# Optimization experiments

Hardware: AMD Instinct MI355X
Metric: run time of the kernel (lower is better)

Reference implementation:

```python
import jax, jax.numpy as jnp
import numpy as np

# Architecture constants (from init_kwargs; reversible halves d_model)
D_MODEL = 1024
D_INNER = D_MODEL // 2          # 512, width of attn/MLP inside reversible block
NUM_HEADS = 8
HEAD_DIM = D_INNER // NUM_HEADS  # 64
SEGMENT_LENGTHS = (512, 1024)
DILATION_RATES = (1, 2)
HIDDEN = 2 * D_INNER             # MLP hidden_layer_multiplier=2


def layer_norm(x, g, b, eps=1e-5):
    m = jnp.mean(x, axis=-1, keepdims=True)
    v = jnp.var(x, axis=-1, keepdims=True)
    return (x - m) * jax.lax.rsqrt(v + eps) * g + b


def dilated_attention(q, k, v):
    """LongNet dilated attention. q,k,v: [b, n, h, dh]. Heads are partitioned
    evenly across (segment_length, dilation_rate) configs; within each config,
    tokens at positions offset::r inside each segment attend to each other."""
    b, n, h, dh = q.shape
    num_groups = len(SEGMENT_LENGTHS)
    gsize = h // num_groups
    scale = 1.0 / np.sqrt(dh).astype(np.float32)
    out = jnp.zeros_like(q)
    for i, (s, r) in enumerate(zip(SEGMENT_LENGTHS, DILATION_RATES)):
        off = i % r
        h0 = i * gsize
        # positions selected by this config: [n_seg, s//r]
        pos = jnp.arange(n // s)[:, None] * s + off + r * jnp.arange(s // r)[None, :]

        def pick(x):
            xs = x[:, :, h0:h0 + gsize, :]      # [b, n, g, dh]
            return xs[:, pos]                   # [b, n_seg, s//r, g, dh]

        qi, ki, vi = pick(q), pick(k), pick(v)
        scores = jnp.einsum('bnqgd,bnkgd->bngqk', qi, ki) * scale
        attn = jax.nn.softmax(scores, axis=-1)
        oi = jnp.einsum('bngqk,bnkgd->bnqgd', attn, vi)
        out = out.at[:, pos.reshape(-1), h0:h0 + gsize, :].set(
            oi.reshape(b, -1, gsize, dh))
    return out


def mhda(x, Wq, bq, Wk, bk, Wv, bv, Wo, bo):
    b, n, d = x.shape
    q = (x @ Wq + bq).reshape(b, n, NUM_HEADS, HEAD_DIM)
    k = (x @ Wk + bk).reshape(b, n, NUM_HEADS, HEAD_DIM)
    v = (x @ Wv + bv).reshape(b, n, NUM_HEADS, HEAD_DIM)
    o = dilated_attention(q, k, v).reshape(b, n, d)
    return o @ Wo + bo


def setup_inputs() -> dict:
    key = jax.random.key(0)
    ks = jax.random.split(key, 8)
    d, hdn = D_INNER, HIDDEN
    w = lambda k, *sh: (jax.random.normal(k, sh, dtype=jnp.float32) * 0.02)
    return {
        'x': jax.random.normal(ks[0], (4, 8192, D_MODEL), dtype=jnp.float32),
        'ln1_g': jnp.ones((d,), jnp.float32), 'ln1_b': jnp.zeros((d,), jnp.float32),
        'Wq': w(ks[1], d, d), 'bq': jnp.zeros((d,), jnp.float32),
        'Wk': w(ks[2], d, d), 'bk': jnp.zeros((d,), jnp.float32),
        'Wv': w(ks[3], d, d), 'bv': jnp.zeros((d,), jnp.float32),
        'Wo': w(ks[4], d, d), 'bo': jnp.zeros((d,), jnp.float32),
        'ln2_g': jnp.ones((d,), jnp.float32), 'ln2_b': jnp.zeros((d,), jnp.float32),
        'W1': w(ks[5], d, hdn), 'b1': jnp.zeros((hdn,), jnp.float32),
        'W2': w(ks[6], hdn, d), 'b2': jnp.zeros((d,), jnp.float32),
    }


def reference(x, ln1_g, ln1_b, Wq, bq, Wk, bk, Wv, bv, Wo, bo,
              ln2_g, ln2_b, W1, b1, W2, b2):
    # Reversible residual block (forward math): split channels in half,
    # y1 = x1 + Attn(LN(x2)); y2 = x2 + MLP(LN(y1)); concat.
    x1, x2 = jnp.split(x, 2, axis=-1)
    y1 = x1 + mhda(layer_norm(x2, ln1_g, ln1_b), Wq, bq, Wk, bk, Wv, bv, Wo, bo)
    h = layer_norm(y1, ln2_g, ln2_b)
    y2 = x2 + jax.nn.relu(h @ W1 + b1) @ W2 + b2
    return jnp.concatenate([y1, y2], axis=-1)
```

## Files before the change

### kernel.cpp

```cpp
#include <hip/hip_runtime.h>
#include <hip/hip_bf16.h>

typedef unsigned short ushort_t;
typedef __bf16 bf16x8 __attribute__((ext_vector_type(8)));
typedef float f32x4 __attribute__((ext_vector_type(4)));
typedef short s16x8 __attribute__((ext_vector_type(8)));

__device__ __forceinline__ float b2f(ushort_t u) {
    union { unsigned u; float f; } x;
    x.u = ((unsigned)u) << 16;
    return x.f;
}
__device__ __forceinline__ ushort_t f2b(float f) {
    union { float f; unsigned u; } x;
    x.f = f;
    unsigned r = x.u + 0x7fffu + ((x.u >> 16) & 1u);
    return (ushort_t)(r >> 16);
}

__device__ __forceinline__ void glds16(const ushort_t* g, ushort_t* l) {
    __builtin_amdgcn_global_load_lds(
        (const __attribute__((address_space(1))) void*)g,
        (__attribute__((address_space(3))) void*)l, 16, 0, 0);
}

__global__ void transpose_k(const float* __restrict__ src, ushort_t* __restrict__ dst,
                            int R, int C) {
    long i = (long)blockIdx.x * 256 + threadIdx.x;
    if (i < (long)R * C) {
        int c = (int)(i / R);
        int r = (int)(i % R);
        dst[i] = f2b(src[(long)r * C + c]);
    }
}

__global__ void concat3_k(const float* a, const float* b, const float* c,
                          float* dst, int n) {
    int i = blockIdx.x * 256 + threadIdx.x;
    if (i < 3 * n) dst[i] = (i < n) ? a[i] : (i < 2 * n ? b[i - n] : c[i - 2 * n]);
}

__global__ __launch_bounds__(256) void ln_kernel(
    const float* __restrict__ x, long xstride,
    const float* __restrict__ g, const float* __restrict__ be,
    ushort_t* __restrict__ out, long ostride) {
    int r = blockIdx.x, t = threadIdx.x;
    const float* row = x + (long)r * xstride;
    float2 p = *(const float2*)(row + 2 * t);
    float v0 = p.x, v1 = p.y;
    float s = v0 + v1, ss = v0 * v0 + v1 * v1;
#pragma unroll
    for (int off = 32; off; off >>= 1) {
        s += __shfl_xor(s, off, 64);
        ss += __shfl_xor(ss, off, 64);
    }
    __shared__ float sb[8];
    int w = t >> 6;
    if ((t & 63) == 0) { sb[w] = s; sb[4 + w] = ss; }
    __syncthreads();
    s = sb[0] + sb[1] + sb[2] + sb[3];
    ss = sb[4] + sb[5] + sb[6] + sb[7];
    float mean = s * (1.f / 512.f);
    float var = ss * (1.f / 512.f) - mean * mean;
    float rstd = rsqrtf(var + 1e-5f);
    float2 gp = *(const float2*)(g + 2 * t);
    float2 bp = *(const float2*)(be + 2 * t);
    ushort2 q;
    q.x = f2b((v0 - mean) * rstd * gp.x + bp.x);
    q.y = f2b((v1 - mean) * rstd * gp.y + bp.y);
    *(ushort2*)(out + (long)r * ostride + 2 * t) = q;
}

__global__ __launch_bounds__(256) void gemm_kernel(
    const ushort_t* __restrict__ A, const ushort_t* __restrict__ Bt,
    const float* __restrict__ bias,
    const float* __restrict__ res, long res_stride,
    void* __restrict__ outp, long out_stride, int out_is_f32,
    int K, int relu) {
    __shared__ __align__(16) ushort_t lA[128 * 32];
    __shared__ __align__(16) ushort_t lB[128 * 32];
    const int t = threadIdx.x;
    const int m0 = blockIdx.x * 128, n0 = blockIdx.y * 128;
    const int wave = t >> 6, lane = t & 63, quad = lane >> 4, l16 = lane & 15;
    const int wm = (wave & 1) * 64, wn = (wave >> 1) * 64;
    f32x4 acc[4][4];
#pragma unroll
    for (int i = 0; i < 4; i++)
#pragma unroll
        for (int j = 0; j < 4; j++) acc[i][j] = (f32x4){0.f, 0.f, 0.f, 0.f};

    const int srow = t >> 2;
    const int scol = (t & 3) * 8;
    const ushort_t* gA0 = A + (long)(m0 + srow) * K + scol;
    const ushort_t* gA1 = gA0 + (long)64 * K;
    const ushort_t* gB0 = Bt + (long)(n0 + srow) * K + scol;
    const ushort_t* gB1 = gB0 + (long)64 * K;
    ushort_t* lA0 = lA + wave * 512;
    ushort_t* lB0 = lB + wave * 512;

    for (int k0 = 0; k0 < K; k0 += 32) {
        __syncthreads();
        glds16(gA0 + k0, lA0);
        glds16(gA1 + k0, lA0 + 2048);
        glds16(gB0 + k0, lB0);
        glds16(gB1 + k0, lB0 + 2048);
        __syncthreads();
        bf16x8 af[4], bfr[4];
#pragma unroll
        for (int i = 0; i < 4; i++) {
            af[i] = *(const bf16x8*)&lA[(wm + i * 16 + l16) * 32 + quad * 8];
            bfr[i] = *(const bf16x8*)&lB[(wn + i * 16 + l16) * 32 + quad * 8];
        }
#pragma unroll
        for (int i = 0; i < 4; i++)
#pragma unroll
            for (int j = 0; j < 4; j++)
                acc[i][j] = __builtin_amdgcn_mfma_f32_16x16x32_bf16(af[i], bfr[j], acc[i][j], 0, 0, 0);
    }
#pragma unroll
    for (int i = 0; i < 4; i++) {
#pragma unroll
        for (int r = 0; r < 4; r++) {
            long row = m0 + wm + i * 16 + quad * 4 + r;
#pragma unroll
            for (int j = 0; j < 4; j++) {
                int col = n0 + wn + j * 16 + l16;
                float v = acc[i][j][r] + bias[col];
                if (res) v += res[row * res_stride + col];
                if (relu) v = fmaxf(v, 0.f);
                if (out_is_f32)
                    ((float*)outp)[row * out_stride + col] = v;
                else
                    ((ushort_t*)outp)[row * out_stride + col] = f2b(v);
            }
        }
    }
}

__global__ __launch_bounds__(256) void attn_kernel(const ushort_t* __restrict__ qkv,
                                                   ushort_t* __restrict__ o) {
    __shared__ __align__(16) ushort_t lK[64 * 72];
    __shared__ __align__(16) ushort_t lV[64 * 72];
    __shared__ __align__(16) ushort_t lP[4 * 32 * 72];

    const int bid = blockIdx.x;
    const int t = threadIdx.x;
    int grp, b, h, seg, qblk;
    if (bid < 1024) {
        grp = 0; qblk = bid & 3; seg = (bid >> 2) & 15; h = (bid >> 6) & 3; b = bid >> 8;
    } else {
        int u = bid - 1024;
        grp = 1; qblk = u & 3; seg = (u >> 2) & 7; h = (u >> 5) & 3; b = u >> 7;
    }
    const int habs = grp * 4 + h;
    const long segbase = (grp == 0) ? (long)seg * 512 : (long)seg * 1024 + 1;
    const int stok = 1 + grp;
    const long btok = (long)b * 8192;
    const int q0 = qblk * 128;

    const int wave = t >> 6, lane = t & 63, quad = lane >> 4, l16 = lane & 15;
    ushort_t* lPw = lP + wave * 32 * 72;

    bf16x8 qf[2][2];
#pragma unroll
    for (int m = 0; m < 2; m++) {
        long tok = btok + segbase + (long)stok * (q0 + wave * 32 + m * 16 + l16);
        const ushort_t* qp = qkv + tok * 1536 + habs * 64;
        qf[m][0] = *(const bf16x8*)(qp + quad * 8);
        qf[m][1] = *(const bf16x8*)(qp + 32 + quad * 8);
    }

    f32x4 oacc[2][4];
#pragma unroll
    for (int m = 0; m < 2; m++)
#pragma unroll
        for (int n = 0; n < 4; n++) oacc[m][n] = (f32x4){0.f, 0.f, 0.f, 0.f};
    float mst[2][4], lst[2][4];
#pragma unroll
    for (int m = 0; m < 2; m++)
#pragma unroll
        for (int r = 0; r < 4; r++) { mst[m][r] = -1e30f; lst[m][r] = 0.f; }

    const int skey = t >> 2;
    const int sdg = t & 3;

    for (int c = 0; c < 8; c++) {
        long ktok = btok + segbase + (long)stok * (c * 64 + skey);
        const ushort_t* kp = qkv + ktok * 1536 + 512 + habs * 64 + sdg * 16;
        s16x8 kr0 = *(const s16x8*)kp;
        s16x8 kr1 = *(const s16x8*)(kp + 8);
        s16x8 vr0 = *(const s16x8*)(kp + 512);
        s16x8 vr1 = *(const s16x8*)(kp + 520);
        __syncthreads();
        *(s16x8*)&lK[skey * 72 + sdg * 16] = kr0;
        *(s16x8*)&lK[skey * 72 + sdg * 16 + 8] = kr1;
#pragma unroll
        for (int i = 0; i < 8; i++) {
            int d0 = sdg * 16 + i, d1 = sdg * 16 + 8 + i;
            lV[d0 * 72 + (skey ^ (((d0 >> 3) & 7) * 8))] = (ushort_t)vr0[i];
            lV[d1 * 72 + (skey ^ (((d1 >> 3) & 7) * 8))] = (ushort_t)vr1[i];
        }
        __syncthreads();

#pragma unroll
        for (int m = 0; m < 2; m++) {
            f32x4 sa[4];
#pragma unroll
            for (int n = 0; n < 4; n++) sa[n] = (f32x4){0.f, 0.f, 0.f, 0.f};
#pragma unroll
            for (int ks = 0; ks < 2; ks++)
#pragma unroll
                for (int n = 0; n < 4; n++) {
                    bf16x8 kf = *(const bf16x8*)&lK[(n * 16 + l16) * 72 + ks * 32 + quad * 8];
                    sa[n] = __builtin_amdgcn_mfma_f32_16x16x32_bf16(qf[m][ks], kf, sa[n], 0, 0, 0);
                }
#pragma unroll
            for (int r = 0; r < 4; r++) {
                float mx = fmaxf(fmaxf(sa[0][r], sa[1][r]), fmaxf(sa[2][r], sa[3][r]));
                mx = fmaxf(mx, __shfl_xor(mx, 1, 64));
                mx = fmaxf(mx, __shfl_xor(mx, 2, 64));
                mx = fmaxf(mx, __shfl_xor(mx, 4, 64));
                mx = fmaxf(mx, __shfl_xor(mx, 8, 64));
                mx *= 0.125f;
                float mold = mst[m][r];
                float mnew = fmaxf(mold, mx);
                float alpha = __expf(mold - mnew);
                float rsum = 0.f;
#pragma unroll
                for (int n = 0; n < 4; n++) {
                    float p = __expf(fmaf(sa[n][r], 0.125f, -mnew));
                    rsum += p;
                    sa[n][r] = p;
                }
                rsum += __shfl_xor(rsum, 1, 64);
                rsum += __shfl_xor(rsum, 2, 64);
                rsum += __shfl_xor(rsum, 4, 64);
                rsum += __shfl_xor(rsum, 8, 64);
                lst[m][r] = lst[m][r] * alpha + rsum;
                mst[m][r] = mnew;
#pragma unroll
                for (int n = 0; n < 4; n++) oacc[m][n][r] *= alpha;
            }
#pragma unroll
            for (int r = 0; r < 4; r++)
#pragma unroll
                for (int n = 0; n < 4; n++)
                    lPw[(m * 16 + quad * 4 + r) * 72 + n * 16 + l16] = f2b(sa[n][r]);
        }
        __asm__ volatile("s_waitcnt lgkmcnt(0)" ::: "memory");

#pragma unroll
        for (int m = 0; m < 2; m++) {
            bf16x8 pf[2];
#pragma unroll
            for (int ks = 0; ks < 2; ks++)
                pf[ks] = *(const bf16x8*)&lPw[(m * 16 + l16) * 72 + ks * 32 + quad * 8];
#pragma unroll
            for (int n = 0; n < 4; n++) {
                int shift = ((n * 2 + (l16 >> 3)) & 7) * 8;
#pragma unroll
                for (int ks = 0; ks < 2; ks++) {
                    int kcol = (ks * 32 + quad * 8) ^ shift;
                    bf16x8 vf = *(const bf16x8*)&lV[(n * 16 + l16) * 72 + kcol];
                    oacc[m][n] = __builtin_amdgcn_mfma_f32_16x16x32_bf16(pf[ks], vf, oacc[m][n], 0, 0, 0);
                }
            }
        }
    }

#pragma unroll
    for (int m = 0; m < 2; m++) {
#pragma unroll
        for (int r = 0; r < 4; r++) {
            float inv = 1.f / lst[m][r];
            long tok = btok + segbase + (long)stok * (q0 + wave * 32 + m * 16 + quad * 4 + r);
            ushort_t* op = o + tok * 512 + habs * 64;
#pragma unroll
            for (int n = 0; n < 4; n++) op[n * 16 + l16] = f2b(oacc[m][n][r] * inv);
        }
    }
}

extern "C" void kernel_launch(void* const* d_in, const int* in_sizes, int n_in,
                              void* d_out, int out_size, void* d_ws, size_t ws_size,
                              hipStream_t stream) {
    const float* x    = (const float*)d_in[0];
    const float* ln1g = (const float*)d_in[1];
    const float* ln1b = (const float*)d_in[2];
    const float* Wq   = (const float*)d_in[3];
    const float* bq   = (const float*)d_in[4];
    const float* Wk   = (const float*)d_in[5];
    const float* bk   = (const float*)d_in[6];
    const float* Wv   = (const float*)d_in[7];
    const float* bv   = (const float*)d_in[8];
    const float* Wo   = (const float*)d_in[9];
    const float* bo   = (const float*)d_in[10];
    const float* ln2g = (const float*)d_in[11];
    const float* ln2b = (const float*)d_in[12];
    const float* W1   = (const float*)d_in[13];
    const float* b1   = (const float*)d_in[14];
    const float* W2   = (const float*)d_in[15];
    const float* b2   = (const float*)d_in[16];
    float* out = (float*)d_out;
    char* ws = (char*)d_ws;

    const size_t NEED = 134217728ull + 1572864 + 524288 + 1048576 + 1048576 + 8192;
    if (ws_size < NEED) return;

    ushort_t* XN    = (ushort_t*)(ws + 0);
    ushort_t* QKV   = (ushort_t*)(ws + 33554432);
    ushort_t* O     = XN;
    ushort_t* H     = XN;
    ushort_t* ACT   = QKV;
    ushort_t* WQKVT = (ushort_t*)(ws + 134217728);
    ushort_t* WOT   = WQKVT + 786432;
    ushort_t* W1T   = WOT + 262144;
    ushort_t* W2T   = W1T + 524288;
    float*    BQKV  = (float*)(W2T + 524288);

    transpose_k<<<1024, 256, 0, stream>>>(Wq, WQKVT, 512, 512);
    transpose_k<<<1024, 256, 0, stream>>>(Wk, WQKVT + 262144, 512, 512);
    transpose_k<<<1024, 256, 0, stream>>>(Wv, WQKVT + 524288, 512, 512);
    transpose_k<<<1024, 256, 0, stream>>>(Wo, WOT, 512, 512);
    transpose_k<<<2048, 256, 0, stream>>>(W1, W1T, 512, 1024);
    transpose_k<<<2048, 256, 0, stream>>>(W2, W2T, 1024, 512);
    concat3_k<<<6, 256, 0, stream>>>(bq, bk, bv, BQKV, 512);

    ln_kernel<<<32768, 256, 0, stream>>>(x + 512, 1024, ln1g, ln1b, XN, 512);
    gemm_kernel<<<dim3(256, 12), 256, 0, stream>>>(XN, WQKVT, BQKV, nullptr, 0,
                                                   QKV, 1536, 0, 512, 0);
    hipMemsetAsync(O, 0, 33554432, stream);
    attn_kernel<<<1536, 256, 0, stream>>>(QKV, O);
    gemm_kernel<<<dim3(256, 4), 256, 0, stream>>>(O, WOT, bo, x, 1024,
                                                  out, 1024, 1, 512, 0);
    ln_kernel<<<32768, 256, 0, stream>>>(out, 1024, ln2g, ln2b, H, 512);
    gemm_kernel<<<dim3(256, 8), 256, 0, stream>>>(H, W1T, b1, nullptr, 0,
                                                  ACT, 1024, 0, 512, 1);
    gemm_kernel<<<dim3(256, 4), 256, 0, stream>>>(ACT, W2T, b2, x + 512, 1024,
                                                  out + 512, 1024, 1, 1024, 0);
}
```

Before: 793.7 us.

## Pipeline GEMM LDS loads with 5-slot ring buffer and vmcnt waits

Replaces the single-buffer load/sync/compute loop in the GEMM kernel with a 5-slot LDS ring. Four K-tiles are prefetched ahead through global_load_lds, and each iteration uses explicit s_waitcnt vmcnt counts plus one barrier. The aim is to hide global memory latency behind MFMA work and to remove one of the two barriers per K step. It raises LDS use to 80KB per block, which may cut occupancy, and it depends on the exact vmcnt bookkeeping being right.

```diff
diff --git a/kernel.cpp b/kernel.cpp
--- a/kernel.cpp
+++ b/kernel.cpp
@@ -77,8 +77,8 @@
     const float* __restrict__ res, long res_stride,
     void* __restrict__ outp, long out_stride, int out_is_f32,
     int K, int relu) {
-    __shared__ __align__(16) ushort_t lA[128 * 32];
-    __shared__ __align__(16) ushort_t lB[128 * 32];
+    __shared__ __align__(16) ushort_t lA[5][128 * 32];
+    __shared__ __align__(16) ushort_t lB[5][128 * 32];
     const int t = threadIdx.x;
     const int m0 = blockIdx.x * 128, n0 = blockIdx.y * 128;
     const int wave = t >> 6, lane = t & 63, quad = lane >> 4, l16 = lane & 15;
@@ -95,21 +95,49 @@
     const ushort_t* gA1 = gA0 + (long)64 * K;
     const ushort_t* gB0 = Bt + (long)(n0 + srow) * K + scol;
     const ushort_t* gB1 = gB0 + (long)64 * K;
-    ushort_t* lA0 = lA + wave * 512;
-    ushort_t* lB0 = lB + wave * 512;
-
-    for (int k0 = 0; k0 < K; k0 += 32) {
-        __syncthreads();
-        glds16(gA0 + k0, lA0);
-        glds16(gA1 + k0, lA0 + 2048);
-        glds16(gB0 + k0, lB0);
-        glds16(gB1 + k0, lB0 + 2048);
-        __syncthreads();
+    const int lofs = wave * 512;
+
+#define ISSUE_TILE(slot, k0)                          \
+    do {                                              \
+        glds16(gA0 + (k0), &lA[slot][lofs]);          \
+        glds16(gA1 + (k0), &lA[slot][lofs + 2048]);   \
+        glds16(gB0 + (k0), &lB[slot][lofs]);          \
+        glds16(gB1 + (k0), &lB[slot][lofs + 2048]);   \
+    } while (0)
+
+    const int T = K >> 5;
+    ISSUE_TILE(0, 0);
+    ISSUE_TILE(1, 32);
+    ISSUE_TILE(2, 64);
+    ISSUE_TILE(3, 96);
+
+    int pr = 0, pw = 4;
+    for (int tt = 0; tt < T; ++tt) {
+        if (tt < T - 3)
+            asm volatile("s_waitcnt vmcnt(12)" ::: "memory");
+        else if (tt == T - 3)
+            asm volatile("s_waitcnt vmcnt(8)" ::: "memory");
+        else if (tt == T - 2)
+            asm volatile("s_waitcnt vmcnt(4)" ::: "memory");
+        else
+            asm volatile("s_waitcnt vmcnt(0)" ::: "memory");
+        __builtin_amdgcn_s_barrier();
+        asm volatile("" ::: "memory");
+
+        if (tt + 4 < T) {
+            ISSUE_TILE(pw, (tt + 4) * 32);
+            pw = (pw == 4) ? 0 : pw + 1;
+        }
+
+        const ushort_t* la = lA[pr];
+        const ushort_t* lb = lB[pr];
+        pr = (pr == 4) ? 0 : pr + 1;
+
         bf16x8 af[4], bfr[4];
 #pragma unroll
         for (int i = 0; i < 4; i++) {
-            af[i] = *(const bf16x8*)&lA[(wm + i * 16 + l16) * 32 + quad * 8];
-            bfr[i] = *(const bf16x8*)&lB[(wn + i * 16 + l16) * 32 + quad * 8];
+            af[i]  = *(const bf16x8*)&la[(wm + i * 16 + l16) * 32 + quad * 8];
+            bfr[i] = *(const bf16x8*)&lb[(wn + i * 16 + l16) * 32 + quad * 8];
         }
 #pragma unroll
         for (int i = 0; i < 4; i++)
@@ -117,6 +145,8 @@
             for (int j = 0; j < 4; j++)
                 acc[i][j] = __builtin_amdgcn_mfma_f32_16x16x32_bf16(af[i], bfr[j], acc[i][j], 0, 0, 0);
     }
+#undef ISSUE_TILE
+
 #pragma unroll
     for (int i = 0; i < 4; i++) {
 #pragma unroll
```

Result: slower. 819.9 us (+3.3%).

## Widen GEMM tiles to 128x512 with double-buffered LDS prefetch

Applied to the files above, without the earlier changes.

The GEMM kernel moves to 512 threads and a 128x512 output tile, with each wave computing a 64x128 sub-tile. Global-to-LDS loads for the next K-step are issued into a second buffer while the current one is consumed, replacing the two barriers per step with one wait and one barrier. This is meant to reuse each A tile across more columns and hide load latency behind MFMA work. In exchange the grid drops to 256-768 blocks, and the 32 accumulators per thread raise register pressure, which may limit occupancy and load balance on a chip with many CUs.

```diff
diff --git a/kernel.cpp b/kernel.cpp
--- a/kernel.cpp
+++ b/kernel.cpp
@@ -71,59 +71,74 @@
     *(ushort2*)(out + (long)r * ostride + 2 * t) = q;
 }
 
-__global__ __launch_bounds__(256) void gemm_kernel(
+__global__ __launch_bounds__(512, 2) void gemm_kernel(
     const ushort_t* __restrict__ A, const ushort_t* __restrict__ Bt,
     const float* __restrict__ bias,
     const float* __restrict__ res, long res_stride,
     void* __restrict__ outp, long out_stride, int out_is_f32,
     int K, int relu) {
-    __shared__ __align__(16) ushort_t lA[128 * 32];
-    __shared__ __align__(16) ushort_t lB[128 * 32];
+    __shared__ __align__(16) ushort_t lA[2][128 * 32];
+    __shared__ __align__(16) ushort_t lB[2][512 * 32];
     const int t = threadIdx.x;
-    const int m0 = blockIdx.x * 128, n0 = blockIdx.y * 128;
+    const int m0 = blockIdx.x * 128, n0 = blockIdx.y * 512;
     const int wave = t >> 6, lane = t & 63, quad = lane >> 4, l16 = lane & 15;
-    const int wm = (wave & 1) * 64, wn = (wave >> 1) * 64;
-    f32x4 acc[4][4];
+    const int wm = (wave & 1) * 64, wn = (wave >> 1) * 128;
+    f32x4 acc[4][8];
 #pragma unroll
     for (int i = 0; i < 4; i++)
 #pragma unroll
-        for (int j = 0; j < 4; j++) acc[i][j] = (f32x4){0.f, 0.f, 0.f, 0.f};
+        for (int j = 0; j < 8; j++) acc[i][j] = (f32x4){0.f, 0.f, 0.f, 0.f};
 
     const int srow = t >> 2;
     const int scol = (t & 3) * 8;
-    const ushort_t* gA0 = A + (long)(m0 + srow) * K + scol;
-    const ushort_t* gA1 = gA0 + (long)64 * K;
+    const ushort_t* gA  = A  + (long)(m0 + srow) * K + scol;
     const ushort_t* gB0 = Bt + (long)(n0 + srow) * K + scol;
-    const ushort_t* gB1 = gB0 + (long)64 * K;
-    ushort_t* lA0 = lA + wave * 512;
-    ushort_t* lB0 = lB + wave * 512;
-
-    for (int k0 = 0; k0 < K; k0 += 32) {
-        __syncthreads();
-        glds16(gA0 + k0, lA0);
-        glds16(gA1 + k0, lA0 + 2048);
-        glds16(gB0 + k0, lB0);
-        glds16(gB1 + k0, lB0 + 2048);
-        __syncthreads();
-        bf16x8 af[4], bfr[4];
-#pragma unroll
-        for (int i = 0; i < 4; i++) {
-            af[i] = *(const bf16x8*)&lA[(wm + i * 16 + l16) * 32 + quad * 8];
-            bfr[i] = *(const bf16x8*)&lB[(wn + i * 16 + l16) * 32 + quad * 8];
-        }
+    const ushort_t* gB1 = gB0 + (long)128 * K;
+    const ushort_t* gB2 = gB0 + (long)256 * K;
+    const ushort_t* gB3 = gB0 + (long)384 * K;
+    const int lofs = wave * 512;
+
+#define ISSUE_TILE(sl, k0)                              \
+    do {                                                \
+        glds16(gA  + (k0), &lA[sl][lofs]);              \
+        glds16(gB0 + (k0), &lB[sl][lofs]);              \
+        glds16(gB1 + (k0), &lB[sl][4096 + lofs]);       \
+        glds16(gB2 + (k0), &lB[sl][8192 + lofs]);       \
+        glds16(gB3 + (k0), &lB[sl][12288 + lofs]);      \
+    } while (0)
+
+    const int T = K >> 5;
+    ISSUE_TILE(0, 0);
+    int sl = 0;
+    for (int tt = 0; tt < T; ++tt) {
+        asm volatile("s_waitcnt vmcnt(0)" ::: "memory");
+        __builtin_amdgcn_s_barrier();
+        asm volatile("" ::: "memory");
+        if (tt + 1 < T) ISSUE_TILE(sl ^ 1, (tt + 1) * 32);
+        const ushort_t* la = lA[sl];
+        const ushort_t* lb = lB[sl];
+        sl ^= 1;
+        bf16x8 af[4];
 #pragma unroll
         for (int i = 0; i < 4; i++)
-#pragma unroll
-            for (int j = 0; j < 4; j++)
-                acc[i][j] = __builtin_amdgcn_mfma_f32_16x16x32_bf16(af[i], bfr[j], acc[i][j], 0, 0, 0);
-    }
+            af[i] = *(const bf16x8*)&la[(wm + i * 16 + l16) * 32 + quad * 8];
+#pragma unroll
+        for (int j = 0; j < 8; j++) {
+            bf16x8 bfv = *(const bf16x8*)&lb[(wn + j * 16 + l16) * 32 + quad * 8];
+#pragma unroll
+            for (int i = 0; i < 4; i++)
+                acc[i][j] = __builtin_amdgcn_mfma_f32_16x16x32_bf16(af[i], bfv, acc[i][j], 0, 0, 0);
+        }
+    }
+#undef ISSUE_TILE
+
 #pragma unroll
     for (int i = 0; i < 4; i++) {
 #pragma unroll
         for (int r = 0; r < 4; r++) {
             long row = m0 + wm + i * 16 + quad * 4 + r;
 #pragma unroll
-            for (int j = 0; j < 4; j++) {
+            for (int j = 0; j < 8; j++) {
                 int col = n0 + wn + j * 16 + l16;
                 float v = acc[i][j][r] + bias[col];
                 if (res) v += res[row * res_stride + col];
@@ -327,15 +342,15 @@
     concat3_k<<<6, 256, 0, stream>>>(bq, bk, bv, BQKV, 512);
 
     ln_kernel<<<32768, 256, 0, stream>>>(x + 512, 1024, ln1g, ln1b, XN, 512);
-    gemm_kernel<<<dim3(256, 12), 256, 0, stream>>>(XN, WQKVT, BQKV, nullptr, 0,
-                                                   QKV, 1536, 0, 512, 0);
+    gemm_kernel<<<dim3(256, 3), 512, 0, stream>>>(XN, WQKVT, BQKV, nullptr, 0,
+                                                  QKV, 1536, 0, 512, 0);
     hipMemsetAsync(O, 0, 33554432, stream);
     attn_kernel<<<1536, 256, 0, stream>>>(QKV, O);
-    gemm_kernel<<<dim3(256, 4), 256, 0, stream>>>(O, WOT, bo, x, 1024,
+    gemm_kernel<<<dim3(256, 1), 512, 0, stream>>>(O, WOT, bo, x, 1024,
                                                   out, 1024, 1, 512, 0);
     ln_kernel<<<32768, 256, 0, stream>>>(out, 1024, ln2g, ln2b, H, 512);
-    gemm_kernel<<<dim3(256, 8), 256, 0, stream>>>(H, W1T, b1, nullptr, 0,
+    gemm_kernel<<<dim3(256, 2), 512, 0, stream>>>(H, W1T, b1, nullptr, 0,
                                                   ACT, 1024, 0, 512, 1);
-    gemm_kernel<<<dim3(256, 4), 256, 0, stream>>>(ACT, W2T, b2, x + 512, 1024,
+    gemm_kernel<<<dim3(256, 1), 512, 0, stream>>>(ACT, W2T, b2, x + 512, 1024,
                                                   out + 512, 1024, 1, 1024, 0);
 }
```

New measurement: 817.8 us. +3.0%, slower.

## Double-buffer GEMM LDS tiles and remap blocks for XCD-local reuse

Applied to the files above, without the earlier changes.

The GEMM kernel now double-buffers its LDS tiles. The global-to-LDS load for the next K step is issued right after the barrier, so it overlaps the MFMA work on the current tile, and the loop needs one barrier per step instead of two. The launch grid is flattened to 1D and block IDs are remapped so that each XCD (bid&7) handles a contiguous run of M tiles and walks all N tiles, which is meant to improve L2 reuse of the A rows. Launch bounds now request 5 waves per SIMD, and LDS use per block doubles to 32KB, which could limit occupancy.

```diff
diff --git a/kernel.cpp b/kernel.cpp
--- a/kernel.cpp
+++ b/kernel.cpp
@@ -71,16 +71,23 @@
     *(ushort2*)(out + (long)r * ostride + 2 * t) = q;
 }
 
-__global__ __launch_bounds__(256) void gemm_kernel(
+__global__ __launch_bounds__(256, 5) void gemm_kernel(
     const ushort_t* __restrict__ A, const ushort_t* __restrict__ Bt,
     const float* __restrict__ bias,
     const float* __restrict__ res, long res_stride,
     void* __restrict__ outp, long out_stride, int out_is_f32,
-    int K, int relu) {
-    __shared__ __align__(16) ushort_t lA[128 * 32];
-    __shared__ __align__(16) ushort_t lB[128 * 32];
+    int K, int relu, int nTiles) {
+    __shared__ __align__(16) ushort_t lA[2][128 * 32];
+    __shared__ __align__(16) ushort_t lB[2][128 * 32];
     const int t = threadIdx.x;
-    const int m0 = blockIdx.x * 128, n0 = blockIdx.y * 128;
+    const int bid = blockIdx.x;
+    const int xcd = bid & 7;
+    const int jj = bid >> 3;
+    const int mPerXcd = (int)gridDim.x / (nTiles * 8);
+    const int mt = xcd * mPerXcd + jj / nTiles;
+    const int nt = jj % nTiles;
+    const int m0 = mt * 128, n0 = nt * 128;
+
     const int wave = t >> 6, lane = t & 63, quad = lane >> 4, l16 = lane & 15;
     const int wm = (wave & 1) * 64, wn = (wave >> 1) * 64;
     f32x4 acc[4][4];
@@ -95,21 +102,32 @@
     const ushort_t* gA1 = gA0 + (long)64 * K;
     const ushort_t* gB0 = Bt + (long)(n0 + srow) * K + scol;
     const ushort_t* gB1 = gB0 + (long)64 * K;
-    ushort_t* lA0 = lA + wave * 512;
-    ushort_t* lB0 = lB + wave * 512;
-
-    for (int k0 = 0; k0 < K; k0 += 32) {
-        __syncthreads();
-        glds16(gA0 + k0, lA0);
-        glds16(gA1 + k0, lA0 + 2048);
-        glds16(gB0 + k0, lB0);
-        glds16(gB1 + k0, lB0 + 2048);
-        __syncthreads();
+    const int lofs = wave * 512;
+
+#define ISSUE_TILE(sl, k0)                             \
+    do {                                               \
+        glds16(gA0 + (k0), &lA[sl][lofs]);             \
+        glds16(gA1 + (k0), &lA[sl][2048 + lofs]);      \
+        glds16(gB0 + (k0), &lB[sl][lofs]);             \
+        glds16(gB1 + (k0), &lB[sl][2048 + lofs]);      \
+    } while (0)
+
+    const int T = K >> 5;
+    ISSUE_TILE(0, 0);
+    int sl = 0;
+    for (int tt = 0; tt < T; ++tt) {
+        asm volatile("s_waitcnt vmcnt(0)" ::: "memory");
+        __builtin_amdgcn_s_barrier();
+        asm volatile("" ::: "memory");
+        if (tt + 1 < T) ISSUE_TILE(sl ^ 1, (tt + 1) * 32);
+        const ushort_t* la = lA[sl];
+        const ushort_t* lb = lB[sl];
+        sl ^= 1;
         bf16x8 af[4], bfr[4];
 #pragma unroll
         for (int i = 0; i < 4; i++) {
-            af[i] = *(const bf16x8*)&lA[(wm + i * 16 + l16) * 32 + quad * 8];
-            bfr[i] = *(const bf16x8*)&lB[(wn + i * 16 + l16) * 32 + quad * 8];
+            af[i]  = *(const bf16x8*)&la[(wm + i * 16 + l16) * 32 + quad * 8];
+            bfr[i] = *(const bf16x8*)&lb[(wn + i * 16 + l16) * 32 + quad * 8];
         }
 #pragma unroll
         for (int i = 0; i < 4; i++)
@@ -117,6 +135,8 @@
             for (int j = 0; j < 4; j++)
                 acc[i][j] = __builtin_amdgcn_mfma_f32_16x16x32_bf16(af[i], bfr[j], acc[i][j], 0, 0, 0);
     }
+#undef ISSUE_TILE
+
 #pragma unroll
     for (int i = 0; i < 4; i++) {
 #pragma unroll
@@ -327,15 +347,15 @@
     concat3_k<<<6, 256, 0, stream>>>(bq, bk, bv, BQKV, 512);
 
     ln_kernel<<<32768, 256, 0, stream>>>(x + 512, 1024, ln1g, ln1b, XN, 512);
-    gemm_kernel<<<dim3(256, 12), 256, 0, stream>>>(XN, WQKVT, BQKV, nullptr, 0,
-                                                   QKV, 1536, 0, 512, 0);
+    gemm_kernel<<<3072, 256, 0, stream>>>(XN, WQKVT, BQKV, nullptr, 0,
+                                          QKV, 1536, 0, 512, 0, 12);
     hipMemsetAsync(O, 0, 33554432, stream);
     attn_kernel<<<1536, 256, 0, stream>>>(QKV, O);
-    gemm_kernel<<<dim3(256, 4), 256, 0, stream>>>(O, WOT, bo, x, 1024,
-                                                  out, 1024, 1, 512, 0);
+    gemm_kernel<<<1024, 256, 0, stream>>>(O, WOT, bo, x, 1024,
+                                          out, 1024, 1, 512, 0, 4);
     ln_kernel<<<32768, 256, 0, stream>>>(out, 1024, ln2g, ln2b, H, 512);
-    gemm_kernel<<<dim3(256, 8), 256, 0, stream>>>(H, W1T, b1, nullptr, 0,
-                                                  ACT, 1024, 0, 512, 1);
-    gemm_kernel<<<dim3(256, 4), 256, 0, stream>>>(ACT, W2T, b2, x + 512, 1024,
-                                                  out + 512, 1024, 1, 1024, 0);
-}
+    gemm_kernel<<<2048, 256, 0, stream>>>(H, W1T, b1, nullptr, 0,
+                                          ACT, 1024, 0, 512, 1, 8);
+    gemm_kernel<<<1024, 256, 0, stream>>>(ACT, W2T, b2, x + 512, 1024,
+                                          out + 512, 1024, 1, 1024, 0, 4);
+}
```

New measurement: 883.6 us. +11.3%, slower.
